# Kernel tuning notes

Measured on AMD Instinct MI355X. Metric: run time of the kernel, lower is better.

Reference implementation:

```python
import jax, jax.numpy as jnp
import numpy as np

B, S, H, NH, K = 8, 1024, 1024, 16, 512
HD = H // NH  # head dim = 64


def setup_inputs() -> dict:
    key = jax.random.key(0)
    ks = jax.random.split(key, 9)
    hidden_states = jax.random.normal(ks[0], (B, S, H), jnp.float32)
    # remain_layers: exactly K nonzero entries per row (static max_tokens = K)
    scores = jax.random.uniform(ks[1], (B, S))
    thresh = jnp.sort(scores, axis=1)[:, S - K][:, None]
    remain_layers = (scores >= thresh).astype(jnp.int32)
    attention_mask = jnp.zeros((B, 1, 1, S), jnp.float32)  # additive mask
    init = 0.02
    Wq = jax.random.normal(ks[2], (H, H), jnp.float32) * init
    bq = jnp.zeros((H,), jnp.float32)
    Wk = jax.random.normal(ks[3], (H, H), jnp.float32) * init
    bk = jnp.zeros((H,), jnp.float32)
    Wv = jax.random.normal(ks[4], (H, H), jnp.float32) * init
    bv = jnp.zeros((H,), jnp.float32)
    return {"hidden_states": hidden_states, "attention_mask": attention_mask,
            "remain_layers": remain_layers, "Wq": Wq, "bq": bq,
            "Wk": Wk, "bk": bk, "Wv": Wv, "bv": bv}


def _heads(x):  # [B, L, H] -> [B, NH, L, HD]
    b, l, _ = x.shape
    return x.reshape(b, l, NH, HD).transpose(0, 2, 1, 3)


def reference(hidden_states, attention_mask, remain_layers, Wq, bq, Wk, bk, Wv, bv):
    # get_reduced_hidden: per-row gather of tokens with remain_layers > 0,
    # in original position order, zero-padded to max_tokens (= K here).
    order = jnp.argsort(1 - remain_layers, axis=1, stable=True)  # nonzeros first, order kept
    idx = order[:, :K]                                           # [B, K]
    reduced = jnp.take_along_axis(hidden_states, idx[:, :, None], axis=1)  # [B, K, H]
    valid = (jnp.take_along_axis(remain_layers, idx, axis=1) > 0)
    reduced = reduced * valid[:, :, None].astype(reduced.dtype)  # zero-pad slots

    q = _heads(reduced @ Wq.T + bq)          # [B, NH, K, HD]
    k = _heads(hidden_states @ Wk.T + bk)    # [B, NH, S, HD]
    v = _heads(hidden_states @ Wv.T + bv)    # [B, NH, S, HD]

    scores = jnp.einsum('bhqd,bhkd->bhqk', q, k) / np.sqrt(HD).astype(np.float32)
    scores = scores + attention_mask         # additive mask broadcast
    probs = jax.nn.softmax(scores, axis=-1)  # dropout is identity at eval
    ctx = jnp.einsum('bhqk,bhkd->bhqd', probs, v)  # [B, NH, K, HD]
    ctx = ctx.transpose(0, 2, 1, 3).reshape(B, K, H)
    return ctx
```

## Files before the change

### kernel.cpp

```cpp
#include <hip/hip_runtime.h>
#include <hip/hip_bf16.h>
#include <stdint.h>

#define S_LEN 1024
#define HDIM  1024
#define NHEADS 16
#define HEAD_D 64
#define KSEL  512
#define BATCH 8

typedef unsigned short ushort_t;
typedef __attribute__((ext_vector_type(8))) __bf16 bf16x8;
typedef __attribute__((ext_vector_type(4))) float  f32x4;

typedef const __attribute__((address_space(1))) void cg_void;
typedef __attribute__((address_space(3))) void lds_void;

__device__ __forceinline__ void gl_lds16(const void* g, void* l) {
    __builtin_amdgcn_global_load_lds((cg_void*)g, (lds_void*)l, 16, 0, 0);
}

__device__ __forceinline__ ushort_t f2bf(float f) {
    union { float f; unsigned int i; } x; x.f = f;
    unsigned int r = (x.i + 0x7fffu + ((x.i >> 16) & 1u)) >> 16;
    return (ushort_t)r;
}

__global__ __launch_bounds__(1024) void prep_kernel(
    const float* __restrict__ hidden, const float* __restrict__ wq,
    const float* __restrict__ wk, const float* __restrict__ wv,
    const int* __restrict__ remain,
    ushort_t* __restrict__ hbf, ushort_t* __restrict__ wqb,
    ushort_t* __restrict__ wkb, ushort_t* __restrict__ wvb,
    int* __restrict__ idx, int* __restrict__ valid) {
    __shared__ int wsum[16];
    __shared__ int woff[17];
    int blk = blockIdx.x;
    if (blk < 2816) {
        const float* s; ushort_t* d; int base;
        if (blk < 2048)      { s = hidden; d = hbf; base = blk; }
        else if (blk < 2304) { s = wq; d = wqb; base = blk - 2048; }
        else if (blk < 2560) { s = wk; d = wkb; base = blk - 2304; }
        else                 { s = wv; d = wvb; base = blk - 2560; }
        int i = base * 1024 + threadIdx.x;
        float4 v = ((const float4*)s)[i];
        ushort4 o;
        o.x = f2bf(v.x); o.y = f2bf(v.y); o.z = f2bf(v.z); o.w = f2bf(v.w);
        ((ushort4*)d)[i] = o;
    } else {
        int b = blk - 2816, t = threadIdx.x;
        int r = remain[b * S_LEN + t];
        unsigned long long m = __ballot(r != 0);
        int lane = t & 63, w = t >> 6;
        int pre = __popcll(m & ((1ull << lane) - 1ull));
        if (lane == 0) wsum[w] = __popcll(m);
        __syncthreads();
        if (t == 0) { int a = 0; for (int i = 0; i < 16; i++) { woff[i] = a; a += wsum[i]; } woff[16] = a; }
        __syncthreads();
        int tot = woff[16];
        int onesBefore = woff[w] + pre;
        int slot = r ? onesBefore : (tot + (t - onesBefore));
        if (slot < KSEL) { idx[b * KSEL + slot] = t; valid[b * KSEL + slot] = r; }
    }
}

#define QSCALE 0.1803368801111244f
#define LT_PITCH 136
__global__ __launch_bounds__(256, 4) void gemm_fused(
    const ushort_t* __restrict__ hbf, const ushort_t* __restrict__ wkv,
    const ushort_t* __restrict__ wq,
    const float* __restrict__ bk, const float* __restrict__ bv,
    const float* __restrict__ bq,
    const int* __restrict__ idx, const int* __restrict__ valid,
    ushort_t* __restrict__ kp, ushort_t* __restrict__ vt, ushort_t* __restrict__ qp) {
    __shared__ __align__(16) ushort_t pool[16384];
    ushort_t* As = pool;
    ushort_t* Bs = pool + 8192;
    const int i = blockIdx.x;
    int z, bmI, bnI;
    if (i < 256) { z = 1; bmI = i >> 3; bnI = i & 7; }
    else         { z = 0; int ii = i - 256; int x = ii & 7, j = ii >> 3;
                   bmI = x * 8 + (j >> 4); bnI = j & 15; }
    const long bm = (long)bmI * 128;
    const int bn = bnI * 128;

    const int tid = threadIdx.x;
    const int lane = tid & 63;
    const int w = tid >> 6;
    const int quad = lane >> 4;
    const int cl = lane & 15;
    const int srow = w * 16 + (lane >> 2);
    const int fs = ((lane >> 2) & 3) ^ ((lane >> 4) & 3);
    const int scol = ((lane & 3) ^ fs) * 8;
    const int lds_off = w * 512 + lane * 8;
    const int wr = (w >> 1) * 64, wc = (w & 1) * 64;
    const int fr = (cl & 3) ^ ((cl >> 2) & 3);
    const int qo = (quad ^ fr) * 8;

    const ushort_t* W = z ? wq : wkv;

    long ab[2];
#pragma unroll
    for (int p = 0; p < 2; p++) {
        long gr = bm + p * 64 + srow;
        if (z == 0) ab[p] = gr * HDIM;
        else {
            int b_ = (int)(gr >> 9);
            int src = idx[(b_ << 9) + ((int)gr & 511)];
            ab[p] = ((long)(b_ << 10) + src) * HDIM;
        }
    }

    f32x4 acc[4][4] = {};

    for (int k0 = 0; k0 < HDIM; k0 += 64) {
#pragma unroll
        for (int p = 0; p < 2; p++)
#pragma unroll
            for (int hh = 0; hh < 2; hh++) {
                gl_lds16(hbf + ab[p] + k0 + hh * 32 + scol, &As[hh * 4096 + p * 2048 + lds_off]);
                gl_lds16(W + ((long)(bn + p * 64 + srow)) * HDIM + k0 + hh * 32 + scol,
                         &Bs[hh * 4096 + p * 2048 + lds_off]);
            }
        __syncthreads();
#pragma unroll
        for (int hh = 0; hh < 2; hh++) {
            bf16x8 af[4], bfr[4];
#pragma unroll
            for (int mt = 0; mt < 4; mt++)
                af[mt] = *(const bf16x8*)&As[hh * 4096 + (wr + mt * 16 + cl) * 32 + qo];
#pragma unroll
            for (int nt = 0; nt < 4; nt++)
                bfr[nt] = *(const bf16x8*)&Bs[hh * 4096 + (wc + nt * 16 + cl) * 32 + qo];
#pragma unroll
            for (int mt = 0; mt < 4; mt++)
#pragma unroll
                for (int nt = 0; nt < 4; nt++)
                    acc[mt][nt] = __builtin_amdgcn_mfma_f32_16x16x32_bf16(af[mt], bfr[nt], acc[mt][nt], 0, 0, 0);
        }
        __syncthreads();
    }

    if (z == 1) {
#pragma unroll
        for (int nt = 0; nt < 4; nt++) {
            int col = bn + wc + nt * 16 + cl;
            float bvq = bq[col];
#pragma unroll
            for (int mt = 0; mt < 4; mt++) {
                long row = bm + wr + mt * 16 + quad * 4;
#pragma unroll
                for (int r = 0; r < 4; r++) {
                    float vm = (float)valid[row + r];
                    qp[(row + r) * HDIM + col] = f2bf((acc[mt][nt][r] * vm + bvq) * QSCALE);
                }
            }
        }
    } else if (bn < 1024) {
#pragma unroll
        for (int nt = 0; nt < 4; nt++) {
            int col = bn + wc + nt * 16 + cl;
            float bvk = bk[col];
#pragma unroll
            for (int mt = 0; mt < 4; mt++) {
                long row = bm + wr + mt * 16 + quad * 4;
#pragma unroll
                for (int r = 0; r < 4; r++)
                    kp[(row + r) * HDIM + col] = f2bf(acc[mt][nt][r] + bvk);
            }
        }
    } else {
        ushort_t* Lt = pool;
        long b_ = bm >> 10, s0 = bm & 1023;
#pragma unroll
        for (int p2 = 0; p2 < 2; p2++) {
            if ((w & 1) == p2) {
#pragma unroll
                for (int nt = 0; nt < 4; nt++) {
                    int cloc = nt * 16 + cl;
                    float bvv = bv[bn - 1024 + p2 * 64 + cloc];
#pragma unroll
                    for (int mt = 0; mt < 4; mt++) {
                        int row0 = wr + mt * 16 + quad * 4;
#pragma unroll
                        for (int r = 0; r < 4; r++)
                            Lt[cloc * LT_PITCH + row0 + r] = f2bf(acc[mt][nt][r] + bvv);
                    }
                }
            }
            __syncthreads();
            int c2 = tid >> 2, quarter = tid & 3;
            long gbase = ((b_ << 10) + (bn - 1024) + p2 * 64 + c2) * 1024 + s0 + quarter * 32;
            const ushort_t* src = Lt + c2 * LT_PITCH + quarter * 32;
#pragma unroll
            for (int q8 = 0; q8 < 4; q8++)
                *(bf16x8*)(vt + gbase + q8 * 8) = *(const bf16x8*)(src + q8 * 8);
            __syncthreads();
        }
    }
}

#define P_PITCH 72
__global__ __launch_bounds__(256, 2) void attn_kernel(
    const ushort_t* __restrict__ qp, const ushort_t* __restrict__ kp,
    const ushort_t* __restrict__ vt, const float* __restrict__ mask,
    float* __restrict__ out) {
    __shared__ __align__(16) ushort_t ks[2][4096];
    __shared__ __align__(16) ushort_t vs[2][4096];
    __shared__ __align__(16) ushort_t ps[4][32 * P_PITCH];
    const int tid = threadIdx.x;
    const int lane = tid & 63;
    const int w = tid >> 6;
    const int quad = lane >> 4;
    const int cl = lane & 15;
    const int qt = blockIdx.x, h = blockIdx.y, b = blockIdx.z;

    const int srow = tid >> 2;
    const int fsa = ((tid >> 2) & 3) ^ ((tid >> 4) & 3);
    const int sc8 = ((tid & 3) ^ fsa) * 8;
    const int lds_off = tid * 8;
    const int fr = (cl & 3) ^ ((cl >> 2) & 3);
    const int qo = (quad ^ fr) * 8;

    const long kbase = (long)b * S_LEN;
    const long vbase = (long)b * 1024 + h * HEAD_D;

    const long qrow0 = (long)b * KSEL + qt * 128 + w * 32;
    bf16x8 aq[2][2];
#pragma unroll
    for (int mt = 0; mt < 2; mt++)
#pragma unroll
        for (int kk = 0; kk < 2; kk++)
            aq[mt][kk] = *(const bf16x8*)(qp + (qrow0 + mt * 16 + cl) * HDIM + h * HEAD_D + kk * 32 + quad * 8);

    f32x4 O[2][4] = {};
    float l_r[2][4] = {};

#pragma unroll
    for (int j = 0; j < 2; j++) {
        gl_lds16(kp + (kbase + srow) * (long)HDIM + h * HEAD_D + j * 32 + sc8, &ks[0][j * 2048 + lds_off]);
        gl_lds16(vt + (vbase + srow) * (long)S_LEN + j * 32 + sc8, &vs[0][j * 2048 + lds_off]);
    }

    for (int c = 0; c < S_LEN / 64; c++) {
        __asm__ volatile("s_waitcnt vmcnt(0)" ::: "memory");
        __syncthreads();
        if (c + 1 < S_LEN / 64) {
            int nb = (c + 1) & 1;
#pragma unroll
            for (int j = 0; j < 2; j++) {
                gl_lds16(kp + (kbase + (c + 1) * 64 + srow) * (long)HDIM + h * HEAD_D + j * 32 + sc8,
                         &ks[nb][j * 2048 + lds_off]);
                gl_lds16(vt + (vbase + srow) * (long)S_LEN + (c + 1) * 64 + j * 32 + sc8,
                         &vs[nb][j * 2048 + lds_off]);
            }
        }
        const ushort_t* kbuf = ks[c & 1];
        const ushort_t* vbuf = vs[c & 1];

        f32x4 sc[2][4] = {};
#pragma unroll
        for (int kk = 0; kk < 2; kk++)
#pragma unroll
            for (int nt = 0; nt < 4; nt++) {
                bf16x8 bk8 = *(const bf16x8*)&kbuf[kk * 2048 + (nt * 16 + cl) * 32 + qo];
#pragma unroll
                for (int mt = 0; mt < 2; mt++)
                    sc[mt][nt] = __builtin_amdgcn_mfma_f32_16x16x32_bf16(aq[mt][kk], bk8, sc[mt][nt], 0, 0, 0);
            }

#pragma unroll
        for (int nt = 0; nt < 4; nt++) {
            float mv = mask[b * S_LEN + c * 64 + nt * 16 + cl] * 1.44269504f;
#pragma unroll
            for (int mt = 0; mt < 2; mt++)
#pragma unroll
                for (int r = 0; r < 4; r++) {
                    float p_ = __builtin_amdgcn_exp2f(sc[mt][nt][r] + mv);
                    sc[mt][nt][r] = p_;
                    l_r[mt][r] += p_;
                }
        }

#pragma unroll
        for (int mt = 0; mt < 2; mt++)
#pragma unroll
            for (int nt = 0; nt < 4; nt++)
#pragma unroll
                for (int r = 0; r < 4; r++)
                    ps[w][(mt * 16 + quad * 4 + r) * P_PITCH + nt * 16 + cl] = f2bf(sc[mt][nt][r]);

        __asm__ volatile("s_waitcnt lgkmcnt(0)" ::: "memory");

#pragma unroll
        for (int kk = 0; kk < 2; kk++) {
            bf16x8 ap[2];
#pragma unroll
            for (int mt = 0; mt < 2; mt++)
                ap[mt] = *(const bf16x8*)&ps[w][(mt * 16 + cl) * P_PITCH + kk * 32 + quad * 8];
#pragma unroll
            for (int dt = 0; dt < 4; dt++) {
                bf16x8 bv8 = *(const bf16x8*)&vbuf[kk * 2048 + (dt * 16 + cl) * 32 + qo];
#pragma unroll
                for (int mt = 0; mt < 2; mt++)
                    O[mt][dt] = __builtin_amdgcn_mfma_f32_16x16x32_bf16(ap[mt], bv8, O[mt][dt], 0, 0, 0);
            }
        }
    }

#pragma unroll
    for (int mt = 0; mt < 2; mt++)
#pragma unroll
        for (int r = 0; r < 4; r++) {
            float s0 = l_r[mt][r];
#pragma unroll
            for (int d = 1; d < 16; d <<= 1) s0 += __shfl_xor(s0, d, 64);
            l_r[mt][r] = s0;
        }

#pragma unroll
    for (int mt = 0; mt < 2; mt++) {
        const long orow0 = qrow0 + mt * 16 + quad * 4;
#pragma unroll
        for (int dt = 0; dt < 4; dt++) {
            int col = h * HEAD_D + dt * 16 + cl;
#pragma unroll
            for (int r = 0; r < 4; r++)
                out[(orow0 + r) * HDIM + col] = O[mt][dt][r] / l_r[mt][r];
        }
    }
}

extern "C" void kernel_launch(void* const* d_in, const int* in_sizes, int n_in,
                              void* d_out, int out_size, void* d_ws, size_t ws_size,
                              hipStream_t stream) {
    const float* hidden = (const float*)d_in[0];
    const float* mask   = (const float*)d_in[1];
    const int*   remain = (const int*)d_in[2];
    const float* Wq = (const float*)d_in[3];
    const float* bq = (const float*)d_in[4];
    const float* Wk = (const float*)d_in[5];
    const float* bk = (const float*)d_in[6];
    const float* Wv = (const float*)d_in[7];
    const float* bv = (const float*)d_in[8];
    float* out = (float*)d_out;

    char* ws = (char*)d_ws;
    size_t off = 0;
    int* idx   = (int*)(ws + off); off += 16384;
    int* valid = (int*)(ws + off); off += 16384;
    ushort_t* hbf = (ushort_t*)(ws + off); off += (size_t)BATCH * S_LEN * HDIM * 2;
    ushort_t* wqb = (ushort_t*)(ws + off); off += (size_t)HDIM * HDIM * 2;
    ushort_t* wkb = (ushort_t*)(ws + off); off += (size_t)HDIM * HDIM * 2;
    ushort_t* wvb = (ushort_t*)(ws + off); off += (size_t)HDIM * HDIM * 2;
    ushort_t* qp  = (ushort_t*)(ws + off); off += (size_t)BATCH * KSEL * HDIM * 2;
    ushort_t* kp  = (ushort_t*)(ws + off); off += (size_t)BATCH * S_LEN * HDIM * 2;
    ushort_t* vt  = (ushort_t*)(ws + off); off += (size_t)BATCH * S_LEN * HDIM * 2;

    prep_kernel<<<2824, 1024, 0, stream>>>(hidden, Wq, Wk, Wv, remain,
                                           hbf, wqb, wkb, wvb, idx, valid);
    gemm_fused<<<1280, 256, 0, stream>>>(hbf, wkb, wqb, bk, bv, bq,
                                         idx, valid, kp, vt, qp);
    attn_kernel<<<dim3(4, NHEADS, BATCH), 256, 0, stream>>>(qp, kp, vt, mask, out);
}
```

Measured before the change: 192.4 us.

## Rewrite QKV GEMM with 256x256 tiles, pipelined staging, and Q computed on all tokens

The fused projection GEMM moves from 128x128 tiles with 256 threads to 256x256 tiles with 512 threads and 128KB of LDS. Global-to-LDS loads are double-buffered and interleaved with MFMA phases using explicit barriers, vmcnt waits and priority hints. Q is now projected over all S tokens as part of one combined K|V|Q weight matrix, and a per-token position map scatters only the selected rows into the Q output, replacing the gathered-row A loads. This trades extra Q FLOPs (double the Q rows) for a single uniform, better-reused GEMM with fewer blocks and better latency hiding.

```diff
diff --git a/kernel.cpp b/kernel.cpp
--- a/kernel.cpp
+++ b/kernel.cpp
@@ -32,7 +32,7 @@
     const int* __restrict__ remain,
     ushort_t* __restrict__ hbf, ushort_t* __restrict__ wqb,
     ushort_t* __restrict__ wkb, ushort_t* __restrict__ wvb,
-    int* __restrict__ idx, int* __restrict__ valid) {
+    short* __restrict__ pos, int* __restrict__ valid) {
     __shared__ int wsum[16];
     __shared__ int woff[17];
     int blk = blockIdx.x;
@@ -60,142 +60,178 @@
         int tot = woff[16];
         int onesBefore = woff[w] + pre;
         int slot = r ? onesBefore : (tot + (t - onesBefore));
-        if (slot < KSEL) { idx[b * KSEL + slot] = t; valid[b * KSEL + slot] = r; }
+        pos[b * S_LEN + t] = (short)((slot < KSEL) ? slot : -1);
+        if (slot < KSEL) valid[b * KSEL + slot] = r;
     }
 }
 
 #define QSCALE 0.1803368801111244f
-#define LT_PITCH 136
-__global__ __launch_bounds__(256, 4) void gemm_fused(
-    const ushort_t* __restrict__ hbf, const ushort_t* __restrict__ wkv,
-    const ushort_t* __restrict__ wq,
+#define LT_PITCH 264
+#define BAR() __asm__ volatile("s_barrier" ::: "memory")
+#define VMCNT(n) __asm__ volatile("s_waitcnt vmcnt(" #n ")" ::: "memory")
+
+#define GPHASE(mt0, ...) { \
+    bf16x8 Af0, Af1, Af2, Af3; \
+    { const ushort_t* ap = &pool[Ab + (mt0) * 1024 + aRow]; \
+      Af0 = *(const bf16x8*)(ap + ksw0); \
+      Af1 = *(const bf16x8*)(ap + ksw1); \
+      Af2 = *(const bf16x8*)(ap + 1024 + ksw0); \
+      Af3 = *(const bf16x8*)(ap + 1024 + ksw1); } \
+    __VA_ARGS__; \
+    BAR(); \
+    __builtin_amdgcn_s_setprio(1); \
+    _Pragma("unroll") for (int nt = 0; nt < 4; nt++) \
+        acc[mt0][nt]   = __builtin_amdgcn_mfma_f32_16x16x32_bf16(Af0, Bf[nt][0], acc[mt0][nt], 0, 0, 0); \
+    _Pragma("unroll") for (int nt = 0; nt < 4; nt++) \
+        acc[mt0+1][nt] = __builtin_amdgcn_mfma_f32_16x16x32_bf16(Af2, Bf[nt][0], acc[mt0+1][nt], 0, 0, 0); \
+    _Pragma("unroll") for (int nt = 0; nt < 4; nt++) \
+        acc[mt0][nt]   = __builtin_amdgcn_mfma_f32_16x16x32_bf16(Af1, Bf[nt][1], acc[mt0][nt], 0, 0, 0); \
+    _Pragma("unroll") for (int nt = 0; nt < 4; nt++) \
+        acc[mt0+1][nt] = __builtin_amdgcn_mfma_f32_16x16x32_bf16(Af3, Bf[nt][1], acc[mt0+1][nt], 0, 0, 0); \
+    __builtin_amdgcn_s_setprio(0); \
+    __builtin_amdgcn_sched_barrier(0); \
+    BAR(); }
+
+__global__ __launch_bounds__(512, 2) void gemm8(
+    const ushort_t* __restrict__ hbf, const ushort_t* __restrict__ wkvq,
     const float* __restrict__ bk, const float* __restrict__ bv,
     const float* __restrict__ bq,
-    const int* __restrict__ idx, const int* __restrict__ valid,
+    const short* __restrict__ pos, const int* __restrict__ valid,
     ushort_t* __restrict__ kp, ushort_t* __restrict__ vt, ushort_t* __restrict__ qp) {
-    __shared__ __align__(16) ushort_t pool[16384];
-    ushort_t* As = pool;
-    ushort_t* Bs = pool + 8192;
+    __shared__ __align__(16) ushort_t pool[65536];
     const int i = blockIdx.x;
-    int z, bmI, bnI;
-    if (i < 256) { z = 1; bmI = i >> 3; bnI = i & 7; }
-    else         { z = 0; int ii = i - 256; int x = ii & 7, j = ii >> 3;
-                   bmI = x * 8 + (j >> 4); bnI = j & 15; }
-    const long bm = (long)bmI * 128;
-    const int bn = bnI * 128;
+    const int swz = (i & 7) * 48 + (i >> 3);
+    const int bmI = swz / 12, bnI = swz % 12;
+    const int bm = bmI * 256;
+    const int bn = bnI * 256;
 
     const int tid = threadIdx.x;
     const int lane = tid & 63;
     const int w = tid >> 6;
     const int quad = lane >> 4;
     const int cl = lane & 15;
-    const int srow = w * 16 + (lane >> 2);
-    const int fs = ((lane >> 2) & 3) ^ ((lane >> 4) & 3);
-    const int scol = ((lane & 3) ^ fs) * 8;
-    const int lds_off = w * 512 + lane * 8;
-    const int wr = (w >> 1) * 64, wc = (w & 1) * 64;
-    const int fr = (cl & 3) ^ ((cl >> 2) & 3);
-    const int qo = (quad ^ fr) * 8;
-
-    const ushort_t* W = z ? wq : wkv;
-
-    long ab[2];
-#pragma unroll
-    for (int p = 0; p < 2; p++) {
-        long gr = bm + p * 64 + srow;
-        if (z == 0) ab[p] = gr * HDIM;
-        else {
-            int b_ = (int)(gr >> 9);
-            int src = idx[(b_ << 9) + ((int)gr & 511)];
-            ab[p] = ((long)(b_ << 10) + src) * HDIM;
-        }
-    }
-
-    f32x4 acc[4][4] = {};
-
-    for (int k0 = 0; k0 < HDIM; k0 += 64) {
-#pragma unroll
-        for (int p = 0; p < 2; p++)
-#pragma unroll
-            for (int hh = 0; hh < 2; hh++) {
-                gl_lds16(hbf + ab[p] + k0 + hh * 32 + scol, &As[hh * 4096 + p * 2048 + lds_off]);
-                gl_lds16(W + ((long)(bn + p * 64 + srow)) * HDIM + k0 + hh * 32 + scol,
-                         &Bs[hh * 4096 + p * 2048 + lds_off]);
-            }
-        __syncthreads();
-#pragma unroll
-        for (int hh = 0; hh < 2; hh++) {
-            bf16x8 af[4], bfr[4];
-#pragma unroll
-            for (int mt = 0; mt < 4; mt++)
-                af[mt] = *(const bf16x8*)&As[hh * 4096 + (wr + mt * 16 + cl) * 32 + qo];
-#pragma unroll
-            for (int nt = 0; nt < 4; nt++)
-                bfr[nt] = *(const bf16x8*)&Bs[hh * 4096 + (wc + nt * 16 + cl) * 32 + qo];
-#pragma unroll
-            for (int mt = 0; mt < 4; mt++)
-#pragma unroll
-                for (int nt = 0; nt < 4; nt++)
-                    acc[mt][nt] = __builtin_amdgcn_mfma_f32_16x16x32_bf16(af[mt], bfr[nt], acc[mt][nt], 0, 0, 0);
-        }
-        __syncthreads();
-    }
-
-    if (z == 1) {
+    const int wr = w >> 2;
+    const int wc = w & 3;
+
+    const int r0 = tid >> 3;
+    const int csw = ((tid & 7) ^ (r0 & 7)) * 8;
+    const ushort_t* aSrc = hbf  + (bm + r0) * 1024 + csw;
+    const ushort_t* bSrc = wkvq + (bn + r0) * 1024 + csw;
+
+    const int aRow = cl * 64;
+    const int ksw0 = (quad ^ (cl & 7)) * 8;
+    const int ksw1 = ksw0 ^ 32;
+    const int BbW = 32768 + (wc & 1) * 4096;
+    const int BhT = wc >> 1;
+
+    auto stageA = [&](int kt, int half) {
+        const ushort_t* s = aSrc + half * 131072 + kt * 64;
+        ushort_t* d = &pool[((kt & 1) * 2 + half) * 8192 + tid * 8];
+        gl_lds16(s, d);
+        gl_lds16(s + 65536, d + 4096);
+    };
+    auto stageB = [&](int kt, int half) {
+        const ushort_t* s = bSrc + half * 131072 + kt * 64;
+        ushort_t* d = &pool[32768 + ((kt & 1) * 2 + half) * 8192 + tid * 8];
+        gl_lds16(s, d);
+        gl_lds16(s + 65536, d + 4096);
+    };
+
+    f32x4 acc[8][4] = {};
+
+    stageA(0, 0); stageA(0, 1);
+    stageB(0, 0); stageB(0, 1);
+    stageB(1, 0); stageB(1, 1);
+    VMCNT(4);
+    BAR();
+
+    for (int u = 0; u < 16; ++u) {
+        const int buf = u & 1;
+        const int Ab = (buf * 2 + wr) * 8192;
+        const int Bb = BbW + (buf * 2 + BhT) * 8192;
+
+        bf16x8 Bf[4][2];
 #pragma unroll
         for (int nt = 0; nt < 4; nt++) {
-            int col = bn + wc + nt * 16 + cl;
-            float bvq = bq[col];
-#pragma unroll
-            for (int mt = 0; mt < 4; mt++) {
-                long row = bm + wr + mt * 16 + quad * 4;
-#pragma unroll
-                for (int r = 0; r < 4; r++) {
-                    float vm = (float)valid[row + r];
-                    qp[(row + r) * HDIM + col] = f2bf((acc[mt][nt][r] * vm + bvq) * QSCALE);
-                }
-            }
-        }
-    } else if (bn < 1024) {
+            const ushort_t* bp = &pool[Bb + nt * 1024 + aRow];
+            Bf[nt][0] = *(const bf16x8*)(bp + ksw0);
+            Bf[nt][1] = *(const bf16x8*)(bp + ksw1);
+        }
+        GPHASE(0, { if (u < 15) { stageA(u + 1, 0); stageA(u + 1, 1); } })
+        GPHASE(2, { if (u < 14) stageB(u + 2, 0); })
+        GPHASE(4, { if (u < 14) stageB(u + 2, 1); })
+        GPHASE(6, { if (u < 14) { VMCNT(4); } else { VMCNT(0); } })
+    }
+
+    const int row0 = bm + wr * 128;
+    const int colW = wc * 64;
+    if (bnI < 4) {
+        const int cb = bn + colW;
 #pragma unroll
         for (int nt = 0; nt < 4; nt++) {
-            int col = bn + wc + nt * 16 + cl;
-            float bvk = bk[col];
-#pragma unroll
-            for (int mt = 0; mt < 4; mt++) {
-                long row = bm + wr + mt * 16 + quad * 4;
+            int col = cb + nt * 16 + cl;
+            float bb = bk[col];
+#pragma unroll
+            for (int mt = 0; mt < 8; mt++) {
+                int rw = row0 + mt * 16 + quad * 4;
 #pragma unroll
                 for (int r = 0; r < 4; r++)
-                    kp[(row + r) * HDIM + col] = f2bf(acc[mt][nt][r] + bvk);
-            }
-        }
-    } else {
-        ushort_t* Lt = pool;
-        long b_ = bm >> 10, s0 = bm & 1023;
+                    kp[(rw + r) * 1024 + col] = f2bf(acc[mt][nt][r] + bb);
+            }
+        }
+    } else if (bnI < 8) {
+        const int vcb = bn - 1024;
+        const int b_ = bm >> 10;
+        const int s0 = bm & 1023;
 #pragma unroll
         for (int p2 = 0; p2 < 2; p2++) {
-            if ((w & 1) == p2) {
+            if ((wc >> 1) == p2) {
 #pragma unroll
                 for (int nt = 0; nt < 4; nt++) {
-                    int cloc = nt * 16 + cl;
-                    float bvv = bv[bn - 1024 + p2 * 64 + cloc];
-#pragma unroll
-                    for (int mt = 0; mt < 4; mt++) {
-                        int row0 = wr + mt * 16 + quad * 4;
+                    int cloc = (wc & 1) * 64 + nt * 16 + cl;
+                    float bb = bv[vcb + p2 * 128 + cloc];
+#pragma unroll
+                    for (int mt = 0; mt < 8; mt++) {
+                        int rr = wr * 128 + mt * 16 + quad * 4;
 #pragma unroll
                         for (int r = 0; r < 4; r++)
-                            Lt[cloc * LT_PITCH + row0 + r] = f2bf(acc[mt][nt][r] + bvv);
+                            pool[cloc * LT_PITCH + rr + r] = f2bf(acc[mt][nt][r] + bb);
                     }
                 }
             }
             __syncthreads();
-            int c2 = tid >> 2, quarter = tid & 3;
-            long gbase = ((b_ << 10) + (bn - 1024) + p2 * 64 + c2) * 1024 + s0 + quarter * 32;
-            const ushort_t* src = Lt + c2 * LT_PITCH + quarter * 32;
-#pragma unroll
-            for (int q8 = 0; q8 < 4; q8++)
-                *(bf16x8*)(vt + gbase + q8 * 8) = *(const bf16x8*)(src + q8 * 8);
+            {
+                int col = tid >> 2;
+                int sq = tid & 3;
+                int gb = ((b_ << 10) + vcb + p2 * 128 + col) * 1024 + s0;
+                const ushort_t* src = &pool[col * LT_PITCH];
+#pragma unroll
+                for (int j = 0; j < 8; j++) {
+                    int ch = (sq + 4 * j) * 8;
+                    *(bf16x8*)(vt + gb + ch) = *(const bf16x8*)(src + ch);
+                }
+            }
             __syncthreads();
+        }
+    } else {
+        const int qcb = bn - 2048 + colW;
+        float bqv[4];
+#pragma unroll
+        for (int nt = 0; nt < 4; nt++) bqv[nt] = bq[qcb + nt * 16 + cl];
+#pragma unroll
+        for (int mt = 0; mt < 8; mt++) {
+#pragma unroll
+            for (int r = 0; r < 4; r++) {
+                int row = row0 + mt * 16 + quad * 4 + r;
+                int p = pos[row];
+                if (p >= 0) {
+                    float vm = (float)valid[((row >> 10) << 9) + p];
+                    int ob = ((row >> 10) * 512 + p) * 1024 + qcb;
+#pragma unroll
+                    for (int nt = 0; nt < 4; nt++)
+                        qp[ob + nt * 16 + cl] = f2bf((acc[mt][nt][r] * vm + bqv[nt]) * QSCALE);
+                }
+            }
         }
     }
 }
@@ -347,19 +383,17 @@
 
     char* ws = (char*)d_ws;
     size_t off = 0;
-    int* idx   = (int*)(ws + off); off += 16384;
+    short* pos   = (short*)(ws + off); off += 16384;
     int* valid = (int*)(ws + off); off += 16384;
-    ushort_t* hbf = (ushort_t*)(ws + off); off += (size_t)BATCH * S_LEN * HDIM * 2;
-    ushort_t* wqb = (ushort_t*)(ws + off); off += (size_t)HDIM * HDIM * 2;
-    ushort_t* wkb = (ushort_t*)(ws + off); off += (size_t)HDIM * HDIM * 2;
-    ushort_t* wvb = (ushort_t*)(ws + off); off += (size_t)HDIM * HDIM * 2;
+    ushort_t* hbf  = (ushort_t*)(ws + off); off += (size_t)BATCH * S_LEN * HDIM * 2;
+    ushort_t* wkvq = (ushort_t*)(ws + off); off += (size_t)3 * HDIM * HDIM * 2;
     ushort_t* qp  = (ushort_t*)(ws + off); off += (size_t)BATCH * KSEL * HDIM * 2;
     ushort_t* kp  = (ushort_t*)(ws + off); off += (size_t)BATCH * S_LEN * HDIM * 2;
     ushort_t* vt  = (ushort_t*)(ws + off); off += (size_t)BATCH * S_LEN * HDIM * 2;
 
     prep_kernel<<<2824, 1024, 0, stream>>>(hidden, Wq, Wk, Wv, remain,
-                                           hbf, wqb, wkb, wvb, idx, valid);
-    gemm_fused<<<1280, 256, 0, stream>>>(hbf, wkb, wqb, bk, bv, bq,
-                                         idx, valid, kp, vt, qp);
+                                           hbf, wkvq + 2 * 1048576, wkvq,
+                                           wkvq + 1048576, pos, valid);
+    gemm8<<<384, 512, 0, stream>>>(hbf, wkvq, bk, bv, bq, pos, valid, kp, vt, qp);
     attn_kernel<<<dim3(4, NHEADS, BATCH), 256, 0, stream>>>(qp, kp, vt, mask, out);
 }
```

Result: slower. 203.9 us (+6.0%).

## Rewrite attention inner loop with transposed 32x32 MFMA and register-resident P

Applied to the files above, without the earlier changes.

The attention kernel switches from 16x16x32 to 32x32x16 bf16 MFMAs. It computes S^T = K·Q^T so each lane holds one query column, which lets the P matrix be converted and repacked in registers with v_cvt_pk_bf16_f32 and v_permlane32_swap rather than round-tripping through shared memory. The mask is preloaded into LDS once per block, outputs are written as float4, and s_setprio wraps the MFMA sections. This removes the per-tile LDS write/read of P and the wait on it, but depends on the new swizzled LDS layout and the permlane mapping being exactly right.

```diff
diff --git a/kernel.cpp b/kernel.cpp
--- a/kernel.cpp
+++ b/kernel.cpp
@@ -12,6 +12,7 @@
 typedef unsigned short ushort_t;
 typedef __attribute__((ext_vector_type(8))) __bf16 bf16x8;
 typedef __attribute__((ext_vector_type(4))) float  f32x4;
+typedef __attribute__((ext_vector_type(16))) float f32x16;
 
 typedef const __attribute__((address_space(1))) void cg_void;
 typedef __attribute__((address_space(3))) void lds_void;
@@ -200,46 +201,48 @@
     }
 }
 
-#define P_PITCH 72
 __global__ __launch_bounds__(256, 2) void attn_kernel(
     const ushort_t* __restrict__ qp, const ushort_t* __restrict__ kp,
     const ushort_t* __restrict__ vt, const float* __restrict__ mask,
     float* __restrict__ out) {
     __shared__ __align__(16) ushort_t ks[2][4096];
     __shared__ __align__(16) ushort_t vs[2][4096];
-    __shared__ __align__(16) ushort_t ps[4][32 * P_PITCH];
+    __shared__ float mlds[1024];
     const int tid = threadIdx.x;
     const int lane = tid & 63;
     const int w = tid >> 6;
-    const int quad = lane >> 4;
-    const int cl = lane & 15;
+    const int ql = lane & 31;
+    const int hi = lane >> 5;
     const int qt = blockIdx.x, h = blockIdx.y, b = blockIdx.z;
 
-    const int srow = tid >> 2;
-    const int fsa = ((tid >> 2) & 3) ^ ((tid >> 4) & 3);
-    const int sc8 = ((tid & 3) ^ fsa) * 8;
-    const int lds_off = tid * 8;
-    const int fr = (cl & 3) ^ ((cl >> 2) & 3);
-    const int qo = (quad ^ fr) * 8;
+    const int sr2 = tid >> 3;
+    const int scS = ((tid & 7) ^ (sr2 & 7)) * 8;
+    const int dOf = tid * 8;
 
     const long kbase = (long)b * S_LEN;
     const long vbase = (long)b * 1024 + h * HEAD_D;
 
+    {
+        float4 mv4 = *(const float4*)(mask + b * S_LEN + tid * 4);
+        mlds[tid * 4 + 0] = mv4.x * 1.44269504f;
+        mlds[tid * 4 + 1] = mv4.y * 1.44269504f;
+        mlds[tid * 4 + 2] = mv4.z * 1.44269504f;
+        mlds[tid * 4 + 3] = mv4.w * 1.44269504f;
+    }
+
     const long qrow0 = (long)b * KSEL + qt * 128 + w * 32;
-    bf16x8 aq[2][2];
-#pragma unroll
-    for (int mt = 0; mt < 2; mt++)
-#pragma unroll
-        for (int kk = 0; kk < 2; kk++)
-            aq[mt][kk] = *(const bf16x8*)(qp + (qrow0 + mt * 16 + cl) * HDIM + h * HEAD_D + kk * 32 + quad * 8);
-
-    f32x4 O[2][4] = {};
-    float l_r[2][4] = {};
+    bf16x8 aq[4];
+#pragma unroll
+    for (int kd = 0; kd < 4; kd++)
+        aq[kd] = *(const bf16x8*)(qp + (qrow0 + ql) * HDIM + h * HEAD_D + kd * 16 + hi * 8);
+
+    f32x16 O[2] = {};
+    float l_loc = 0.f;
 
 #pragma unroll
     for (int j = 0; j < 2; j++) {
-        gl_lds16(kp + (kbase + srow) * (long)HDIM + h * HEAD_D + j * 32 + sc8, &ks[0][j * 2048 + lds_off]);
-        gl_lds16(vt + (vbase + srow) * (long)S_LEN + j * 32 + sc8, &vs[0][j * 2048 + lds_off]);
+        gl_lds16(kp + (kbase + j * 32 + sr2) * (long)HDIM + h * HEAD_D + scS, &ks[0][j * 2048 + dOf]);
+        gl_lds16(vt + (vbase + j * 32 + sr2) * (long)S_LEN + scS, &vs[0][j * 2048 + dOf]);
     }
 
     for (int c = 0; c < S_LEN / 64; c++) {
@@ -249,86 +252,86 @@
             int nb = (c + 1) & 1;
 #pragma unroll
             for (int j = 0; j < 2; j++) {
-                gl_lds16(kp + (kbase + (c + 1) * 64 + srow) * (long)HDIM + h * HEAD_D + j * 32 + sc8,
-                         &ks[nb][j * 2048 + lds_off]);
-                gl_lds16(vt + (vbase + srow) * (long)S_LEN + (c + 1) * 64 + j * 32 + sc8,
-                         &vs[nb][j * 2048 + lds_off]);
-            }
-        }
-        const ushort_t* kbuf = ks[c & 1];
-        const ushort_t* vbuf = vs[c & 1];
-
-        f32x4 sc[2][4] = {};
-#pragma unroll
-        for (int kk = 0; kk < 2; kk++)
-#pragma unroll
-            for (int nt = 0; nt < 4; nt++) {
-                bf16x8 bk8 = *(const bf16x8*)&kbuf[kk * 2048 + (nt * 16 + cl) * 32 + qo];
-#pragma unroll
-                for (int mt = 0; mt < 2; mt++)
-                    sc[mt][nt] = __builtin_amdgcn_mfma_f32_16x16x32_bf16(aq[mt][kk], bk8, sc[mt][nt], 0, 0, 0);
-            }
-
-#pragma unroll
-        for (int nt = 0; nt < 4; nt++) {
-            float mv = mask[b * S_LEN + c * 64 + nt * 16 + cl] * 1.44269504f;
-#pragma unroll
-            for (int mt = 0; mt < 2; mt++)
-#pragma unroll
-                for (int r = 0; r < 4; r++) {
-                    float p_ = __builtin_amdgcn_exp2f(sc[mt][nt][r] + mv);
-                    sc[mt][nt][r] = p_;
-                    l_r[mt][r] += p_;
+                gl_lds16(kp + (kbase + (c + 1) * 64 + j * 32 + sr2) * (long)HDIM + h * HEAD_D + scS,
+                         &ks[nb][j * 2048 + dOf]);
+                gl_lds16(vt + (vbase + j * 32 + sr2) * (long)S_LEN + (c + 1) * 64 + scS,
+                         &vs[nb][j * 2048 + dOf]);
+            }
+        }
+        const ushort_t* kb_ = ks[c & 1];
+        const ushort_t* vb_ = vs[c & 1];
+
+        f32x16 sc[2] = {};
+        __builtin_amdgcn_s_setprio(1);
+#pragma unroll
+        for (int kd = 0; kd < 4; kd++)
+#pragma unroll
+            for (int mtk = 0; mtk < 2; mtk++) {
+                int row = mtk * 32 + ql;
+                bf16x8 af = *(const bf16x8*)&kb_[row * 64 + (((kd * 2 + hi) ^ (row & 7)) * 8)];
+                sc[mtk] = __builtin_amdgcn_mfma_f32_32x32x16_bf16(af, aq[kd], sc[mtk], 0, 0, 0);
+            }
+        __builtin_amdgcn_s_setprio(0);
+
+#pragma unroll
+        for (int mtk = 0; mtk < 2; mtk++)
+#pragma unroll
+            for (int g = 0; g < 4; g++) {
+                f32x4 m4 = *(const f32x4*)&mlds[c * 64 + mtk * 32 + g * 8 + hi * 4];
+#pragma unroll
+                for (int j = 0; j < 4; j++) {
+                    float p_ = __builtin_amdgcn_exp2f(sc[mtk][g * 4 + j] + m4[j]);
+                    sc[mtk][g * 4 + j] = p_;
+                    l_loc += p_;
                 }
-        }
-
-#pragma unroll
-        for (int mt = 0; mt < 2; mt++)
-#pragma unroll
-            for (int nt = 0; nt < 4; nt++)
-#pragma unroll
-                for (int r = 0; r < 4; r++)
-                    ps[w][(mt * 16 + quad * 4 + r) * P_PITCH + nt * 16 + cl] = f2bf(sc[mt][nt][r]);
-
-        __asm__ volatile("s_waitcnt lgkmcnt(0)" ::: "memory");
-
-#pragma unroll
-        for (int kk = 0; kk < 2; kk++) {
-            bf16x8 ap[2];
-#pragma unroll
-            for (int mt = 0; mt < 2; mt++)
-                ap[mt] = *(const bf16x8*)&ps[w][(mt * 16 + cl) * P_PITCH + kk * 32 + quad * 8];
-#pragma unroll
-            for (int dt = 0; dt < 4; dt++) {
-                bf16x8 bv8 = *(const bf16x8*)&vbuf[kk * 2048 + (dt * 16 + cl) * 32 + qo];
-#pragma unroll
-                for (int mt = 0; mt < 2; mt++)
-                    O[mt][dt] = __builtin_amdgcn_mfma_f32_16x16x32_bf16(ap[mt], bv8, O[mt][dt], 0, 0, 0);
-            }
-        }
-    }
-
-#pragma unroll
-    for (int mt = 0; mt < 2; mt++)
-#pragma unroll
-        for (int r = 0; r < 4; r++) {
-            float s0 = l_r[mt][r];
-#pragma unroll
-            for (int d = 1; d < 16; d <<= 1) s0 += __shfl_xor(s0, d, 64);
-            l_r[mt][r] = s0;
-        }
-
-#pragma unroll
-    for (int mt = 0; mt < 2; mt++) {
-        const long orow0 = qrow0 + mt * 16 + quad * 4;
-#pragma unroll
-        for (int dt = 0; dt < 4; dt++) {
-            int col = h * HEAD_D + dt * 16 + cl;
-#pragma unroll
-            for (int r = 0; r < 4; r++)
-                out[(orow0 + r) * HDIM + col] = O[mt][dt][r] / l_r[mt][r];
-        }
-    }
+            }
+
+        bf16x8 pa[4];
+#pragma unroll
+        for (int mtk = 0; mtk < 2; mtk++)
+#pragma unroll
+            for (int sub = 0; sub < 2; sub++) {
+                unsigned a0, a1, b0, b1;
+                __asm__("v_cvt_pk_bf16_f32 %0, %1, %2" : "=v"(a0)
+                        : "v"(sc[mtk][sub * 8 + 0]), "v"(sc[mtk][sub * 8 + 1]));
+                __asm__("v_cvt_pk_bf16_f32 %0, %1, %2" : "=v"(a1)
+                        : "v"(sc[mtk][sub * 8 + 2]), "v"(sc[mtk][sub * 8 + 3]));
+                __asm__("v_cvt_pk_bf16_f32 %0, %1, %2" : "=v"(b0)
+                        : "v"(sc[mtk][sub * 8 + 4]), "v"(sc[mtk][sub * 8 + 5]));
+                __asm__("v_cvt_pk_bf16_f32 %0, %1, %2" : "=v"(b1)
+                        : "v"(sc[mtk][sub * 8 + 6]), "v"(sc[mtk][sub * 8 + 7]));
+                __asm__("v_permlane32_swap_b32 %0, %1" : "+v"(a0), "+v"(b0));
+                __asm__("v_permlane32_swap_b32 %0, %1" : "+v"(a1), "+v"(b1));
+                union { unsigned u[4]; bf16x8 v; } fr;
+                fr.u[0] = a0; fr.u[1] = a1; fr.u[2] = b0; fr.u[3] = b1;
+                pa[mtk * 2 + sub] = fr.v;
+            }
+
+        __builtin_amdgcn_s_setprio(1);
+#pragma unroll
+        for (int ks_ = 0; ks_ < 4; ks_++)
+#pragma unroll
+            for (int ntd = 0; ntd < 2; ntd++) {
+                int row = ntd * 32 + ql;
+                bf16x8 bvf = *(const bf16x8*)&vb_[row * 64 + (((ks_ * 2 + hi) ^ (row & 7)) * 8)];
+                O[ntd] = __builtin_amdgcn_mfma_f32_32x32x16_bf16(bvf, pa[ks_], O[ntd], 0, 0, 0);
+            }
+        __builtin_amdgcn_s_setprio(0);
+    }
+
+    l_loc += __shfl_xor(l_loc, 32, 64);
+
+#pragma unroll
+    for (int ntd = 0; ntd < 2; ntd++)
+#pragma unroll
+        for (int g = 0; g < 4; g++) {
+            float4 o4;
+            o4.x = O[ntd][g * 4 + 0] / l_loc;
+            o4.y = O[ntd][g * 4 + 1] / l_loc;
+            o4.z = O[ntd][g * 4 + 2] / l_loc;
+            o4.w = O[ntd][g * 4 + 3] / l_loc;
+            *(float4*)(out + (qrow0 + ql) * HDIM + h * HEAD_D + ntd * 32 + g * 8 + hi * 4) = o4;
+        }
 }
 
 extern "C" void kernel_launch(void* const* d_in, const int* in_sizes, int n_in,
```

After: 190.4 us. About the same (-1.0%).
